# Optimization experiments

Measured on AMD Instinct MI355X. Metric: run time of the kernel, lower is better.

## Reference

```python
import jax, jax.numpy as jnp
import numpy as np

SEQ_LEN = 8192
IN = 180      # input_size * window_size = 6 * 30
HID = 64
OUT = 10      # forecast_steps
HPM_H = 2
HPM_IN = OUT + 2 * HID + IN  # 318


def setup_inputs() -> dict:
    key = jax.random.key(0)
    ks = jax.random.split(key, 16)
    u = lambda k, shape, s: jax.random.uniform(k, shape, jnp.float32, -s, s)
    s0 = 1.0 / np.sqrt(HID)
    return {
        "input": jax.random.normal(ks[0], (SEQ_LEN, 1, IN), jnp.float32),
        "W_ih0": u(ks[1], (4 * HID, IN), s0),
        "W_hh0": u(ks[2], (4 * HID, HID), s0),
        "b_ih0": u(ks[3], (4 * HID,), s0),
        "b_hh0": u(ks[4], (4 * HID,), s0),
        "W_ih1": u(ks[5], (4 * HID, HID), s0),
        "W_hh1": u(ks[6], (4 * HID, HID), s0),
        "b_ih1": u(ks[7], (4 * HID,), s0),
        "b_hh1": u(ks[8], (4 * HID,), s0),
        "W_lin": u(ks[9], (OUT, HID), s0),
        "b_lin": u(ks[10], (OUT,), s0),
        "W_h1": u(ks[11], (HPM_H, HPM_IN), 1.0 / np.sqrt(HPM_IN)),
        "b_h1": u(ks[12], (HPM_H,), 1.0 / np.sqrt(HPM_IN)),
        "W_h2": u(ks[13], (IN, HPM_H), 1.0 / np.sqrt(HPM_H)),
        "b_h2": u(ks[14], (IN,), 1.0 / np.sqrt(HPM_H)),
    }


def _lstm_cell(x, h, c, Wih, Whh, bih, bhh):
    g = x @ Wih.T + bih + h @ Whh.T + bhh
    i, f, gg, o = jnp.split(g, 4, axis=-1)
    c2 = jax.nn.sigmoid(f) * c + jax.nn.sigmoid(i) * jnp.tanh(gg)
    h2 = jax.nn.sigmoid(o) * jnp.tanh(c2)
    return h2, c2


def _minmax(x):
    mn = jnp.min(x, axis=0)
    mx = jnp.max(x, axis=0)
    return (x - mn) / (mx - mn + 1e-6)


def reference(input, W_ih0, W_hh0, b_ih0, b_hh0, W_ih1, W_hh1, b_ih1, b_hh1,
              W_lin, b_lin, W_h1, b_h1, W_h2, b_h2):
    S, B, _ = input.shape  # B must be 1 (module structurally requires it)
    z = jnp.zeros((B, HID), input.dtype)

    def step(carry, x):
        h0, c0, h1, c1 = carry
        old_h = h0  # h_t0 before update (old_hts)
        h0, c0 = _lstm_cell(x, h0, c0, W_ih0, W_hh0, b_ih0, b_hh0)
        h1, c1 = _lstm_cell(h0, h1, c1, W_ih1, W_hh1, b_ih1, b_hh1)
        out = h1 @ W_lin.T + b_lin
        return (h0, c0, h1, c1), (out, old_h)

    _, (outs, old_hts) = jax.lax.scan(step, (z, z, z, z), input)
    outputs = outs[:, 0, :]                      # (S, OUT)
    old_hts_n = _minmax(old_hts[:, 0, :])        # (S, HID)
    # mc_dropout=False path: output_hiddens and out_xs are all zeros
    hiddens = jnp.zeros((S, HID), input.dtype)   # min-max of zeros is zeros
    output_data = jnp.concatenate(
        [outputs, hiddens, input[:, 0, :], old_hts_n], axis=1)  # (S, 318)

    def neg_hpm(X):  # F = out_xs - G = -G since out_xs == 0
        return -(jnp.tanh(X @ W_h1.T + b_h1) @ W_h2.T + b_h2)

    F, vjp = jax.vjp(neg_hpm, output_data)       # (S, IN)
    AllF_x = vjp(jnp.ones_like(F))[0]            # grad of sum(F) wrt output_data, (S, 318)
    return outputs, F, AllF_x
```

## Files before the change

kernel.cpp:

```cpp
#include <hip/hip_runtime.h>
#include <hip/hip_bf16.h>
#include <float.h>

#define SEQ   8192
#define INW   180
#define HID   64
#define G4    256
#define OUTW  10
#define XW    318

typedef float f32x4 __attribute__((ext_vector_type(4)));
typedef _Float16 h16x2 __attribute__((ext_vector_type(2)));
typedef unsigned int uint32;

__device__ __forceinline__ float frcp(float x)   { return __builtin_amdgcn_rcpf(x); }
__device__ __forceinline__ float tanhf_f(float x){ return 1.0f - 2.0f * frcp(1.0f + __expf(2.0f * x)); }
__device__ __forceinline__ float gate_act(float x, bool isg) {
    float xx = isg ? 2.0f * x : x;
    float s  = frcp(1.0f + __expf(-xx));
    return isg ? 2.0f * s - 1.0f : s;
}

template<int CTRL>
__device__ __forceinline__ float dpp_bcast(float x) {
    return __int_as_float(__builtin_amdgcn_update_dpp(
        0, __float_as_int(x), CTRL, 0xF, 0xF, true));
}

__device__ __forceinline__ float fdot2h(h16x2 a, h16x2 b, float c) {
#if __has_builtin(__builtin_amdgcn_fdot2)
    return __builtin_amdgcn_fdot2(a, b, c, false);
#else
    asm("v_dot2_f32_f16 %0, %1, %2, %3" : "=v"(c) : "v"(a), "v"(b), "0"(c));
    return c;
#endif
}

__device__ __forceinline__ h16x2 h2f(float f)   { return __builtin_bit_cast(h16x2, f); }
__device__ __forceinline__ h16x2 h2u(uint32 u)  { return __builtin_bit_cast(h16x2, u); }
__device__ __forceinline__ uint32 pack_h2(float lo, float hi) {
    h16x2 h; h.x = (_Float16)lo; h.y = (_Float16)hi;
    return __builtin_bit_cast(uint32, h);
}

__device__ __forceinline__ f32x4 opaque_load4(const float* p) {
    f32x4 v;
    asm volatile("global_load_dwordx4 %0, %1, off" : "=v"(v) : "v"(p));
    return v;
}

__global__ __launch_bounds__(256) void k_packw(
    const float* __restrict__ Whh0, const float* __restrict__ Wih1,
    const float* __restrict__ Whh1,
    uint32* __restrict__ w0h, uint32* __restrict__ w1ah, uint32* __restrict__ w1bh)
{
    const int gid = blockIdx.x * 256 + threadIdx.x;
    const int mat = gid >> 13;
    const int i   = gid & 8191;
    const int r   = i >> 5, k2 = i & 31;
    const float* S = (mat == 0) ? Whh0 : (mat == 1) ? Wih1 : Whh1;
    uint32*      D = (mat == 0) ? w0h  : (mat == 1) ? w1ah : w1bh;
    D[i] = pack_h2(S[r * 64 + 2 * k2], S[r * 64 + 2 * k2 + 1]);
}

#define PRE_TS 16
__global__ __launch_bounds__(256) void k_precompute(
    const float* __restrict__ x, const float* __restrict__ Wih0,
    const float* __restrict__ bih0, const float* __restrict__ bhh0,
    float* __restrict__ pre)
{
    __shared__ float xT[INW][PRE_TS];
    const int t  = threadIdx.x;
    const int rr = (t & 3) * 64 + (t >> 2);
    const int s0 = blockIdx.x * PRE_TS;
    for (int i = t; i < PRE_TS * INW; i += 256) {
        int s = i / INW, k = i % INW;
        xT[k][s] = x[s0 * INW + i];
    }
    __syncthreads();
    float acc[PRE_TS];
    const float b = bih0[rr] + bhh0[rr];
#pragma unroll
    for (int s = 0; s < PRE_TS; ++s) acc[s] = b;
    for (int k = 0; k < INW; ++k) {
        float w = Wih0[rr * INW + k];
#pragma unroll
        for (int s = 0; s < PRE_TS; ++s) acc[s] += w * xT[k][s];
    }
#pragma unroll
    for (int s = 0; s < PRE_TS; ++s) pre[(s0 + s) * G4 + t] = acc[s];
}

#define DOT4(A0, A1, A2, A3, WQ, HQ)                         \
    A0 = fdot2h(h2f((WQ).x), h2u((HQ).x), A0);               \
    A1 = fdot2h(h2f((WQ).y), h2u((HQ).y), A1);               \
    A2 = fdot2h(h2f((WQ).z), h2u((HQ).z), A2);               \
    A3 = fdot2h(h2f((WQ).w), h2u((HQ).w), A3);

__global__ __launch_bounds__(768) __attribute__((amdgpu_waves_per_eu(3, 3)))
void k_lstm_seq(
    const float* __restrict__ pre,
    const uint32* __restrict__ w0h,
    const uint32* __restrict__ w1ah,
    const uint32* __restrict__ w1bh,
    const float* __restrict__ bih1, const float* __restrict__ bhh1,
    float* __restrict__ oldh, float* __restrict__ h1h)
{
    const int t = threadIdx.x;

    __shared__ __attribute__((aligned(16))) uint32 h0p[2][32];
    __shared__ __attribute__((aligned(16))) uint32 h1p[2][32];
    if (t < 32) { h0p[0][t] = 0u; h0p[1][t] = 0u; h1p[0][t] = 0u; h1p[1][t] = 0u; }
    if (t < 64) oldh[t] = 0.0f;
    __syncthreads();

    if (t < 256) {
        const int q = t, g = q & 3, u = q >> 2, r = g * 64 + u;
        const bool isg = (g == 2);

        f32x4 w[8];
        {
            const float* W = (const float*)(w0h + r * 32);
#pragma unroll
            for (int j = 0; j < 8; ++j) w[j] = opaque_load4(W + 4 * j);
            asm volatile("s_waitcnt vmcnt(0)" ::: "memory");
        }
        float c0 = 0.f;
        float preval = pre[q];
        for (int s = 0; s <= SEQ; ++s) {
            if (s < SEQ) {
                const int p = s & 1, pn = p ^ 1;
                const int sn = (s + 1 < SEQ) ? (s + 1) : s;
                float prenext = pre[sn * G4 + q];

                const uint4* Hp = (const uint4*)&h0p[p][0];
                float a0 = preval, a1 = 0.f, a2 = 0.f, a3 = 0.f;
                {
                    uint4 hq0 = Hp[0], hq1 = Hp[1], hq2 = Hp[2], hq3 = Hp[3];
                    DOT4(a0, a1, a2, a3, w[0], hq0)
                    DOT4(a0, a1, a2, a3, w[1], hq1)
                    DOT4(a0, a1, a2, a3, w[2], hq2)
                    DOT4(a0, a1, a2, a3, w[3], hq3)
                }
                __builtin_amdgcn_sched_barrier(0);
                {
                    uint4 hq4 = Hp[4], hq5 = Hp[5], hq6 = Hp[6], hq7 = Hp[7];
                    DOT4(a0, a1, a2, a3, w[4], hq4)
                    DOT4(a0, a1, a2, a3, w[5], hq5)
                    DOT4(a0, a1, a2, a3, w[6], hq6)
                    DOT4(a0, a1, a2, a3, w[7], hq7)
                }
                float a  = gate_act((a0 + a1) + (a2 + a3), isg);
                float ai = dpp_bcast<0x00>(a);
                float af = dpp_bcast<0x55>(a);
                float ag = dpp_bcast<0xAA>(a);
                float ao = dpp_bcast<0xFF>(a);
                c0 = fmaf(af, c0, ai * ag);
                float h0n = ao * tanhf_f(c0);
                float hpart = __shfl_xor(h0n, 4);
                if ((q & 7) == 0) h0p[pn][u >> 1] = pack_h2(h0n, hpart);
                if ((q & 3) == 1 && s + 1 < SEQ) oldh[(s + 1) * HID + u] = h0n;
                preval = prenext;
            }
            asm volatile("s_waitcnt lgkmcnt(0)" ::: "memory");
            __builtin_amdgcn_s_barrier();
            asm volatile("" ::: "memory");
        }
    } else {
        const int i9   = t - 256;
        const int q    = i9 >> 1;
        const int half = i9 & 1;
        const int g    = q & 3, u = q >> 2, r = g * 64 + u;
        const int lane = t & 63;
        const bool isg = (g == 2);
        const bool hi4 = (lane & 4) != 0;

        f32x4 w[8];
        {
            const uint32* Wb = half ? (w1bh + r * 32) : (w1ah + r * 32);
            const float* W = (const float*)Wb;
#pragma unroll
            for (int j = 0; j < 8; ++j) w[j] = opaque_load4(W + 4 * j);
            asm volatile("s_waitcnt vmcnt(0)" ::: "memory");
        }
        const float b1 = bih1[r] + bhh1[r];
        float c1 = 0.f;
        for (int s = 0; s <= SEQ; ++s) {
            if (s >= 1) {
                const int p = s & 1, pn = p ^ 1;

                const uint4* Hp = half ? (const uint4*)&h1p[p][0]
                                       : (const uint4*)&h0p[p][0];
                float a0 = half ? 0.f : b1, a1 = 0.f, a2 = 0.f, a3 = 0.f;
                {
                    uint4 hq0 = Hp[0], hq1 = Hp[1], hq2 = Hp[2], hq3 = Hp[3];
                    DOT4(a0, a1, a2, a3, w[0], hq0)
                    DOT4(a0, a1, a2, a3, w[1], hq1)
                    DOT4(a0, a1, a2, a3, w[2], hq2)
                    DOT4(a0, a1, a2, a3, w[3], hq3)
                }
                __builtin_amdgcn_sched_barrier(0);
                {
                    uint4 hq4 = Hp[4], hq5 = Hp[5], hq6 = Hp[6], hq7 = Hp[7];
                    DOT4(a0, a1, a2, a3, w[4], hq4)
                    DOT4(a0, a1, a2, a3, w[5], hq5)
                    DOT4(a0, a1, a2, a3, w[6], hq6)
                    DOT4(a0, a1, a2, a3, w[7], hq7)
                }
                float ap = (a0 + a1) + (a2 + a3);
                ap += __shfl_xor(ap, 1);
                float a  = gate_act(ap, isg);
                float p0 = dpp_bcast<0x00>(a), p2 = dpp_bcast<0xAA>(a);
                float s0 = __shfl_xor(p0, 4), s2 = __shfl_xor(p2, 4);
                float i_ = hi4 ? s0 : p0, f_ = hi4 ? s2 : p2;
                float g_ = hi4 ? p0 : s0, o_ = hi4 ? p2 : s2;
                c1 = fmaf(f_, c1, i_ * g_);
                float h1n = o_ * tanhf_f(c1);
                float hpart = __shfl_xor(h1n, 8);
                if ((i9 & 15) == 0) h1p[pn][u >> 1] = pack_h2(h1n, hpart);
                if ((i9 & 7) == 2) h1h[(s - 1) * HID + u] = h1n;
            }
            asm volatile("s_waitcnt lgkmcnt(0)" ::: "memory");
            __builtin_amdgcn_s_barrier();
            asm volatile("" ::: "memory");
        }
    }
}

__global__ __launch_bounds__(256) void k_minmax1(
    const float* __restrict__ oldh, float* __restrict__ pmn, float* __restrict__ pmx)
{
    const int t = threadIdx.x, b = blockIdx.x;
    float vmn = FLT_MAX, vmx = -FLT_MAX;
    for (int i = t; i < 128 * HID; i += 256) {
        float v = oldh[b * 128 * HID + i];
        vmn = fminf(vmn, v); vmx = fmaxf(vmx, v);
    }
    __shared__ float smn[256], smx[256];
    smn[t] = vmn; smx[t] = vmx;
    __syncthreads();
    if (t < 64) {
        float m0 = fminf(fminf(smn[t], smn[t + 64]), fminf(smn[t + 128], smn[t + 192]));
        float m1 = fmaxf(fmaxf(smx[t], smx[t + 64]), fmaxf(smx[t + 128], smx[t + 192]));
        pmn[b * 64 + t] = m0; pmx[b * 64 + t] = m1;
    }
}

__global__ __launch_bounds__(256) void k_minmax2(
    const float* __restrict__ pmn, const float* __restrict__ pmx,
    float* __restrict__ mn, float* __restrict__ mx)
{
    const int t = threadIdx.x, col = t & 63, chunk = t >> 6;
    float vmn = FLT_MAX, vmx = -FLT_MAX;
    for (int r = chunk * 16; r < chunk * 16 + 16; ++r) {
        vmn = fminf(vmn, pmn[r * 64 + col]);
        vmx = fmaxf(vmx, pmx[r * 64 + col]);
    }
    __shared__ float smn[256], smx[256];
    smn[t] = vmn; smx[t] = vmx;
    __syncthreads();
    if (t < 64) {
        mn[t] = fminf(fminf(smn[t], smn[t + 64]), fminf(smn[t + 128], smn[t + 192]));
        mx[t] = fmaxf(fmaxf(smx[t], smx[t + 64]), fmaxf(smx[t + 128], smx[t + 192]));
    }
}

__global__ __launch_bounds__(256) void k_finalize(
    const float* __restrict__ h1h, const float* __restrict__ oldh,
    const float* __restrict__ x,
    const float* __restrict__ Wlin, const float* __restrict__ blin,
    const float* __restrict__ Wh1,  const float* __restrict__ bh1,
    const float* __restrict__ Wh2,  const float* __restrict__ bh2,
    const float* __restrict__ mn,   const float* __restrict__ mx,
    float* __restrict__ dout)
{
    float* out_o = dout;
    float* out_F = dout + SEQ * OUTW;
    float* out_A = dout + SEQ * (OUTW + INW);

    const int wave = threadIdx.x >> 6, lane = threadIdx.x & 63;
    const int row  = blockIdx.x * 4 + wave;

    __shared__ float Xs[4][XW + 2];
    __shared__ float h1sh[4][HID];

    h1sh[wave][lane] = h1h[row * HID + lane];
    float mnv = mn[lane], mxv = mx[lane];
    Xs[wave][254 + lane] = (oldh[row * HID + lane] - mnv) * frcp(mxv - mnv + 1e-6f);
    Xs[wave][10 + lane]  = 0.0f;
    for (int c = lane; c < INW; c += 64) Xs[wave][74 + c] = x[row * INW + c];
    __syncthreads();

    if (lane < OUTW) {
        float o = blin[lane];
#pragma unroll
        for (int k = 0; k < HID; ++k) o += Wlin[lane * HID + k] * h1sh[wave][k];
        Xs[wave][lane] = o;
        out_o[row * OUTW + lane] = o;
    }
    __syncthreads();

    float z0 = 0.f, z1 = 0.f, s0 = 0.f, s1 = 0.f;
    for (int c = lane; c < XW; c += 64) {
        float xv = Xs[wave][c];
        z0 += xv * Wh1[c];
        z1 += xv * Wh1[XW + c];
    }
    for (int j = lane; j < INW; j += 64) {
        s0 += Wh2[j * 2 + 0];
        s1 += Wh2[j * 2 + 1];
    }
#pragma unroll
    for (int off = 32; off; off >>= 1) {
        z0 += __shfl_xor(z0, off); z1 += __shfl_xor(z1, off);
        s0 += __shfl_xor(s0, off); s1 += __shfl_xor(s1, off);
    }
    const float t0 = tanhf_f(z0 + bh1[0]);
    const float t1 = tanhf_f(z1 + bh1[1]);
    const float a0 = -s0 * (1.0f - t0 * t0);
    const float a1 = -s1 * (1.0f - t1 * t1);

    for (int c = lane; c < INW; c += 64)
        out_F[row * INW + c] = -(t0 * Wh2[c * 2 + 0] + t1 * Wh2[c * 2 + 1] + bh2[c]);
    for (int c = lane; c < XW; c += 64)
        out_A[row * XW + c] = a0 * Wh1[c] + a1 * Wh1[XW + c];
}

extern "C" void kernel_launch(void* const* d_in, const int* in_sizes, int n_in,
                              void* d_out, int out_size, void* d_ws, size_t ws_size,
                              hipStream_t stream)
{
    const float* input = (const float*)d_in[0];
    const float* Wih0  = (const float*)d_in[1];
    const float* Whh0  = (const float*)d_in[2];
    const float* bih0  = (const float*)d_in[3];
    const float* bhh0  = (const float*)d_in[4];
    const float* Wih1  = (const float*)d_in[5];
    const float* Whh1  = (const float*)d_in[6];
    const float* bih1  = (const float*)d_in[7];
    const float* bhh1  = (const float*)d_in[8];
    const float* Wlin  = (const float*)d_in[9];
    const float* blin  = (const float*)d_in[10];
    const float* Wh1   = (const float*)d_in[11];
    const float* bh1   = (const float*)d_in[12];
    const float* Wh2   = (const float*)d_in[13];
    const float* bh2   = (const float*)d_in[14];

    float* ws   = (float*)d_ws;
    float* pre  = ws;
    float* oldh = pre  + SEQ * G4;
    float* h1h  = oldh + SEQ * HID;
    float* pmn  = h1h  + SEQ * HID;
    float* pmx  = pmn  + 64 * 64;
    float* mn   = pmx  + 64 * 64;
    float* mx   = mn   + 64;
    uint32* w0h  = (uint32*)(mx + 64);
    uint32* w1ah = w0h  + G4 * 32;
    uint32* w1bh = w1ah + G4 * 32;
    float* out  = (float*)d_out;

    hipLaunchKernelGGL(k_packw, dim3(96), dim3(256), 0, stream,
                       Whh0, Wih1, Whh1, w0h, w1ah, w1bh);
    hipLaunchKernelGGL(k_precompute, dim3(SEQ / PRE_TS), dim3(256), 0, stream,
                       input, Wih0, bih0, bhh0, pre);
    hipLaunchKernelGGL(k_lstm_seq, dim3(1), dim3(768), 0, stream,
                       pre, w0h, w1ah, w1bh, bih1, bhh1, oldh, h1h);
    hipLaunchKernelGGL(k_minmax1, dim3(64), dim3(256), 0, stream, oldh, pmn, pmx);
    hipLaunchKernelGGL(k_minmax2, dim3(1), dim3(256), 0, stream, pmn, pmx, mn, mx);
    hipLaunchKernelGGL(k_finalize, dim3(SEQ / 4), dim3(256), 0, stream,
                       h1h, oldh, input, Wlin, blin, Wh1, bh1, Wh2, bh2, mn, mx, out);
}
```

Before: 4.919 ms.

## Give each layer-1 LSTM gate row one thread instead of two halves

Layer-1 work in the sequential LSTM kernel is now done by 256 threads, not 512. Each thread holds both the W_ih1 and W_hh1 row halves in registers and computes the full 128-wide dot product itself. This removes the cross-lane shuffle that combined the partial sums and the extra shuffles used to gather gates, and the block shrinks from 768 to 512 threads, so fewer waves take part in each per-step barrier. In exchange, each thread runs a longer serial dot-product chain and needs more registers (a VGPR count is pinned), which could lengthen the per-step critical path.

```diff
diff --git a/kernel.cpp b/kernel.cpp
--- a/kernel.cpp
+++ b/kernel.cpp
@@ -97,7 +97,7 @@
     A2 = fdot2h(h2f((WQ).z), h2u((HQ).z), A2);               \
     A3 = fdot2h(h2f((WQ).w), h2u((HQ).w), A3);
 
-__global__ __launch_bounds__(768) __attribute__((amdgpu_waves_per_eu(3, 3)))
+__global__ __launch_bounds__(512) __attribute__((amdgpu_num_vgpr(168)))
 void k_lstm_seq(
     const float* __restrict__ pre,
     const uint32* __restrict__ w0h,
@@ -167,20 +167,17 @@
             asm volatile("" ::: "memory");
         }
     } else {
-        const int i9   = t - 256;
-        const int q    = i9 >> 1;
-        const int half = i9 & 1;
-        const int g    = q & 3, u = q >> 2, r = g * 64 + u;
-        const int lane = t & 63;
+        const int q = t - 256, g = q & 3, u = q >> 2, r = g * 64 + u;
         const bool isg = (g == 2);
-        const bool hi4 = (lane & 4) != 0;
-
-        f32x4 w[8];
+
+        f32x4 wa[8], wb[8];
         {
-            const uint32* Wb = half ? (w1bh + r * 32) : (w1ah + r * 32);
-            const float* W = (const float*)Wb;
-#pragma unroll
-            for (int j = 0; j < 8; ++j) w[j] = opaque_load4(W + 4 * j);
+            const float* Wa = (const float*)(w1ah + r * 32);
+            const float* Wb = (const float*)(w1bh + r * 32);
+#pragma unroll
+            for (int j = 0; j < 8; ++j) wa[j] = opaque_load4(Wa + 4 * j);
+#pragma unroll
+            for (int j = 0; j < 8; ++j) wb[j] = opaque_load4(Wb + 4 * j);
             asm volatile("s_waitcnt vmcnt(0)" ::: "memory");
         }
         const float b1 = bih1[r] + bhh1[r];
@@ -188,37 +185,50 @@
         for (int s = 0; s <= SEQ; ++s) {
             if (s >= 1) {
                 const int p = s & 1, pn = p ^ 1;
-
-                const uint4* Hp = half ? (const uint4*)&h1p[p][0]
-                                       : (const uint4*)&h0p[p][0];
-                float a0 = half ? 0.f : b1, a1 = 0.f, a2 = 0.f, a3 = 0.f;
-                {
-                    uint4 hq0 = Hp[0], hq1 = Hp[1], hq2 = Hp[2], hq3 = Hp[3];
-                    DOT4(a0, a1, a2, a3, w[0], hq0)
-                    DOT4(a0, a1, a2, a3, w[1], hq1)
-                    DOT4(a0, a1, a2, a3, w[2], hq2)
-                    DOT4(a0, a1, a2, a3, w[3], hq3)
+                const uint4* H0 = (const uint4*)&h0p[p][0];
+                const uint4* H1 = (const uint4*)&h1p[p][0];
+                float a0 = b1, a1 = 0.f, a2 = 0.f, a3 = 0.f;
+                {
+                    uint4 hq0 = H0[0], hq1 = H0[1], hq2 = H0[2], hq3 = H0[3];
+                    DOT4(a0, a1, a2, a3, wa[0], hq0)
+                    DOT4(a0, a1, a2, a3, wa[1], hq1)
+                    DOT4(a0, a1, a2, a3, wa[2], hq2)
+                    DOT4(a0, a1, a2, a3, wa[3], hq3)
                 }
                 __builtin_amdgcn_sched_barrier(0);
                 {
-                    uint4 hq4 = Hp[4], hq5 = Hp[5], hq6 = Hp[6], hq7 = Hp[7];
-                    DOT4(a0, a1, a2, a3, w[4], hq4)
-                    DOT4(a0, a1, a2, a3, w[5], hq5)
-                    DOT4(a0, a1, a2, a3, w[6], hq6)
-                    DOT4(a0, a1, a2, a3, w[7], hq7)
-                }
-                float ap = (a0 + a1) + (a2 + a3);
-                ap += __shfl_xor(ap, 1);
-                float a  = gate_act(ap, isg);
-                float p0 = dpp_bcast<0x00>(a), p2 = dpp_bcast<0xAA>(a);
-                float s0 = __shfl_xor(p0, 4), s2 = __shfl_xor(p2, 4);
-                float i_ = hi4 ? s0 : p0, f_ = hi4 ? s2 : p2;
-                float g_ = hi4 ? p0 : s0, o_ = hi4 ? p2 : s2;
-                c1 = fmaf(f_, c1, i_ * g_);
-                float h1n = o_ * tanhf_f(c1);
-                float hpart = __shfl_xor(h1n, 8);
-                if ((i9 & 15) == 0) h1p[pn][u >> 1] = pack_h2(h1n, hpart);
-                if ((i9 & 7) == 2) h1h[(s - 1) * HID + u] = h1n;
+                    uint4 hq4 = H0[4], hq5 = H0[5], hq6 = H0[6], hq7 = H0[7];
+                    DOT4(a0, a1, a2, a3, wa[4], hq4)
+                    DOT4(a0, a1, a2, a3, wa[5], hq5)
+                    DOT4(a0, a1, a2, a3, wa[6], hq6)
+                    DOT4(a0, a1, a2, a3, wa[7], hq7)
+                }
+                __builtin_amdgcn_sched_barrier(0);
+                {
+                    uint4 hq0 = H1[0], hq1 = H1[1], hq2 = H1[2], hq3 = H1[3];
+                    DOT4(a0, a1, a2, a3, wb[0], hq0)
+                    DOT4(a0, a1, a2, a3, wb[1], hq1)
+                    DOT4(a0, a1, a2, a3, wb[2], hq2)
+                    DOT4(a0, a1, a2, a3, wb[3], hq3)
+                }
+                __builtin_amdgcn_sched_barrier(0);
+                {
+                    uint4 hq4 = H1[4], hq5 = H1[5], hq6 = H1[6], hq7 = H1[7];
+                    DOT4(a0, a1, a2, a3, wb[4], hq4)
+                    DOT4(a0, a1, a2, a3, wb[5], hq5)
+                    DOT4(a0, a1, a2, a3, wb[6], hq6)
+                    DOT4(a0, a1, a2, a3, wb[7], hq7)
+                }
+                float a  = gate_act((a0 + a1) + (a2 + a3), isg);
+                float ai = dpp_bcast<0x00>(a);
+                float af = dpp_bcast<0x55>(a);
+                float ag = dpp_bcast<0xAA>(a);
+                float ao = dpp_bcast<0xFF>(a);
+                c1 = fmaf(af, c1, ai * ag);
+                float h1n = ao * tanhf_f(c1);
+                float hpart = __shfl_xor(h1n, 4);
+                if ((q & 7) == 0) h1p[pn][u >> 1] = pack_h2(h1n, hpart);
+                if ((q & 3) == 1) h1h[(s - 1) * HID + u] = h1n;
             }
             asm volatile("s_waitcnt lgkmcnt(0)" ::: "memory");
             __builtin_amdgcn_s_barrier();
@@ -363,7 +373,7 @@
                        Whh0, Wih1, Whh1, w0h, w1ah, w1bh);
     hipLaunchKernelGGL(k_precompute, dim3(SEQ / PRE_TS), dim3(256), 0, stream,
                        input, Wih0, bih0, bhh0, pre);
-    hipLaunchKernelGGL(k_lstm_seq, dim3(1), dim3(768), 0, stream,
+    hipLaunchKernelGGL(k_lstm_seq, dim3(1), dim3(512), 0, stream,
                        pre, w0h, w1ah, w1bh, bih1, bhh1, oldh, h1h);
     hipLaunchKernelGGL(k_minmax1, dim3(64), dim3(256), 0, stream, oldh, pmn, pmx);
     hipLaunchKernelGGL(k_minmax2, dim3(1), dim3(256), 0, stream, pmn, pmx, mn, mx);
```

Result: faster. 4.313 ms (-12.3%).
